# Kernel tuning notes

Measured on AMD Instinct MI355X. Metric: run time of the kernel, lower is better.

Reference implementation:

```python
import jax, jax.numpy as jnp
import numpy as np

B, G, T = 4096, 100, 24


def _greedy_dispatch(demand, caps, prices, slack_price):
    """Exact LP solution of: min prices@alloc + slack_price*slack
    s.t. 0<=alloc<=caps, sum(alloc)+slack = demand (per b,t).
    demand: [B,T] (nonneg), caps: [B,G,T], prices: [G], slack_price: scalar.
    Returns alloc [B,G,T], slack [B,T].
    """
    prices_all = jnp.concatenate([prices, slack_price[None]])        # [G+1]
    # slack capacity = demand itself (slack alone can absorb everything)
    caps_all = jnp.concatenate([caps, demand[:, None, :]], axis=1)    # [B,G+1,T]
    order = jnp.argsort(prices_all)                                   # merit order
    caps_s = caps_all[:, order, :]
    before = jnp.cumsum(caps_s, axis=1) - caps_s                      # capacity ahead in merit order
    alloc_s = jnp.clip(demand[:, None, :] - before, 0.0, caps_s)
    inv = jnp.argsort(order)
    alloc = alloc_s[:, inv, :]
    return alloc[:, :-1, :], alloc[:, -1, :]


def setup_inputs() -> dict:
    key = jax.random.key(0)
    k1, k2, k3, k4 = jax.random.split(key, 4)
    R_up = jax.random.uniform(k1, (B, G, T), dtype=jnp.float32)
    R_dn = jax.random.uniform(k2, (B, G, T), dtype=jnp.float32)
    omega_true = jax.random.normal(k3, (B, T), dtype=jnp.float32) * 5.0
    b_G = 10.0 + 40.0 * jax.random.uniform(k4, (G,), dtype=jnp.float32)  # marginal costs $/MWh
    return {
        "R_up": R_up,
        "R_dn": R_dn,
        "omega_true": omega_true,
        "b_G": b_G,
        "voll": jnp.float32(1000.0),
        "vosp": jnp.float32(500.0),
        "rt_up_ratio": jnp.float32(1.5),
        "rt_dn_ratio": jnp.float32(1.2),
    }


def reference(R_up, R_dn, omega_true, b_G, voll, vosp, rt_up_ratio, rt_dn_ratio):
    c_up = rt_up_ratio * b_G                                          # [G]
    c_dn = rt_dn_ratio * b_G                                          # [G]
    dem_up = jnp.maximum(omega_true, 0.0)                             # [B,T]
    dem_dn = jnp.maximum(-omega_true, 0.0)
    du, LS = _greedy_dispatch(dem_up, R_up, c_up, voll)
    dd, SP = _greedy_dispatch(dem_dn, R_dn, c_dn, vosp)
    rt_obj = (jnp.einsum('g,bgt->b', c_up, du)
              + jnp.einsum('g,bgt->b', c_dn, dd)
              + voll * LS.sum(axis=1) + vosp * SP.sum(axis=1))        # [B]
    return du, dd, LS, SP, rt_obj
```

## Files before the change

### kernel.cpp

```cpp
#include <hip/hip_runtime.h>

#define G_ 100
#define T_ 24
#define GP1 101
#define TILE (G_ * T_)
#define VPB (TILE / 4)
#define BLOCK 256
#define WPB 4

typedef float vfloat4 __attribute__((ext_vector_type(4)));

__global__ void setup_sort_kernel(const float* __restrict__ b_G,
                                  const float* __restrict__ voll,
                                  const float* __restrict__ vosp,
                                  const float* __restrict__ ru,
                                  const float* __restrict__ rd,
                                  int* __restrict__ order_out,
                                  float* __restrict__ price_out)
{
    __shared__ float pu[GP1], pd[GP1];
    int i = threadIdx.x;
    if (i < GP1) {
        if (i < G_) { float bg = b_G[i]; pu[i] = ru[0] * bg; pd[i] = rd[0] * bg; }
        else        { pu[i] = voll[0];   pd[i] = vosp[0]; }
    }
    __syncthreads();
    if (i < GP1) {
        float mu = pu[i], md = pd[i];
        int r0 = 0, r1 = 0;
        for (int j = 0; j < GP1; ++j) {
            float vu = pu[j], vd = pd[j];
            r0 += (vu < mu) || (vu == mu && j < i);
            r1 += (vd < md) || (vd == md && j < i);
        }
        order_out[r0] = i;        price_out[r0] = mu;
        order_out[GP1 + r1] = i;  price_out[GP1 + r1] = md;
    }
}

template<int N>
__device__ __forceinline__ void scan_chunk(int k0,
    float* __restrict__ tile, const int* __restrict__ ordp,
    const float* __restrict__ prp, float dem,
    float& before, float& objp, float& slackv)
{
    int gg[N]; float pr[N], cap[N];
#pragma unroll
    for (int j = 0; j < N; ++j) { gg[j] = ordp[k0 + j]; pr[j] = prp[k0 + j]; }
#pragma unroll
    for (int j = 0; j < N; ++j) {
        int gl = (gg[j] < G_) ? gg[j] : 0;
        cap[j] = tile[gl * T_];
    }
#pragma unroll
    for (int j = 0; j < N; ++j) {
        float c = (gg[j] == G_) ? dem : cap[j];
        float a = fminf(fmaxf(dem - before, 0.f), c);
        before += c;
        objp = fmaf(pr[j], a, objp);
        if (gg[j] == G_) slackv = a;
        else             tile[gg[j] * T_] = a;
    }
}

__global__ __launch_bounds__(BLOCK, 4) void dispatch_kernel(
    const float* __restrict__ R_up, const float* __restrict__ R_dn,
    const float* __restrict__ omega,
    const int* __restrict__ ord_ws, const float* __restrict__ pr_ws,
    float* __restrict__ out, int B)
{
    __shared__ float s_tile[WPB * TILE];

    const int tid  = threadIdx.x;
    const int w    = tid >> 6;
    const int lane = tid & 63;
    const int b    = __builtin_amdgcn_readfirstlane(blockIdx.x * WPB + w);
    const size_t bgt = (size_t)B * TILE;
    float* __restrict__ tw = &s_tile[w * TILE];

    vfloat4 buf[10];
    {
        const vfloat4* __restrict__ s0 = (const vfloat4*)R_up + (size_t)b * VPB;
#pragma unroll
        for (int j = 0; j < 9; ++j) buf[j] = s0[lane + j * 64];
        if (lane < VPB - 576) buf[9] = s0[lane + 576];
    }
    float om = 0.f;
    if (lane < T_) om = omega[(size_t)b * T_ + lane];

    float objsum = 0.f;
#pragma unroll
    for (int p = 0; p < 2; ++p) {
#pragma unroll
        for (int j = 0; j < 9; ++j) *(vfloat4*)&tw[(lane + j * 64) * 4] = buf[j];
        if (lane < VPB - 576)       *(vfloat4*)&tw[(lane + 576) * 4]    = buf[9];
        __builtin_amdgcn_wave_barrier();

        if (p == 0) {
            const vfloat4* __restrict__ s1 = (const vfloat4*)R_dn + (size_t)b * VPB;
#pragma unroll
            for (int j = 0; j < 9; ++j) buf[j] = s1[lane + j * 64];
            if (lane < VPB - 576) buf[9] = s1[lane + 576];
        }

        float objp = 0.f;
        if (lane < T_) {
            const float dem = p ? fmaxf(-om, 0.f) : fmaxf(om, 0.f);
            float* __restrict__ tile = tw + lane;
            const int*   __restrict__ ordp = ord_ws + p * GP1;
            const float* __restrict__ prp  = pr_ws  + p * GP1;
            float before = 0.f, slackv = 0.f;
            scan_chunk<16>( 0, tile, ordp, prp, dem, before, objp, slackv);
            scan_chunk<16>(16, tile, ordp, prp, dem, before, objp, slackv);
            scan_chunk<16>(32, tile, ordp, prp, dem, before, objp, slackv);
            scan_chunk<16>(48, tile, ordp, prp, dem, before, objp, slackv);
            scan_chunk<16>(64, tile, ordp, prp, dem, before, objp, slackv);
            scan_chunk<16>(80, tile, ordp, prp, dem, before, objp, slackv);
            scan_chunk< 5>(96, tile, ordp, prp, dem, before, objp, slackv);
            out[2 * bgt + (size_t)p * B * T_ + (size_t)b * T_ + lane] = slackv;
        }
        __builtin_amdgcn_wave_barrier();

#pragma unroll
        for (int off = 32; off; off >>= 1) objp += __shfl_xor(objp, off, 64);
        objsum += objp;

        {
            vfloat4* __restrict__ dst = (vfloat4*)out + ((size_t)p * B + b) * VPB;
#pragma unroll
            for (int j = 0; j < 9; ++j)
                dst[lane + j * 64] = *(const vfloat4*)&tw[(lane + j * 64) * 4];
            if (lane < VPB - 576)
                dst[lane + 576] = *(const vfloat4*)&tw[(lane + 576) * 4];
        }
        __builtin_amdgcn_wave_barrier();
    }

    if (lane == 0)
        out[2 * bgt + 2 * (size_t)B * T_ + b] = objsum;
}

extern "C" void kernel_launch(void* const* d_in, const int* in_sizes, int n_in,
                              void* d_out, int out_size, void* d_ws, size_t ws_size,
                              hipStream_t stream)
{
    const float* R_up  = (const float*)d_in[0];
    const float* R_dn  = (const float*)d_in[1];
    const float* omega = (const float*)d_in[2];
    const float* b_G   = (const float*)d_in[3];
    const float* voll  = (const float*)d_in[4];
    const float* vosp  = (const float*)d_in[5];
    const float* ru    = (const float*)d_in[6];
    const float* rd    = (const float*)d_in[7];

    const int B = in_sizes[0] / TILE;
    float* out = (float*)d_out;

    int*   ord_ws = (int*)d_ws;
    float* pr_ws  = (float*)((char*)d_ws + 2 * GP1 * sizeof(int));

    setup_sort_kernel<<<1, 128, 0, stream>>>(b_G, voll, vosp, ru, rd, ord_ws, pr_ws);

    dispatch_kernel<<<B / WPB, BLOCK, 0, stream>>>(
        R_up, R_dn, omega, ord_ws, pr_ws, out, B);
}
```

Before: 172.5 us.

## Process up and down dispatch concurrently in one wave per batch

```diff
diff --git a/kernel.cpp b/kernel.cpp
--- a/kernel.cpp
+++ b/kernel.cpp
@@ -5,8 +5,6 @@
 #define GP1 101
 #define TILE (G_ * T_)
 #define VPB (TILE / 4)
-#define BLOCK 256
-#define WPB 4
 
 typedef float vfloat4 __attribute__((ext_vector_type(4)));
 
@@ -40,17 +38,24 @@
 
 template<int N>
 __device__ __forceinline__ void scan_chunk(int k0,
-    float* __restrict__ tile, const int* __restrict__ ordp,
-    const float* __restrict__ prp, float dem,
-    float& before, float& objp, float& slackv)
+    const float* __restrict__ lds, int p, int t,
+    const int* __restrict__ o0, const int* __restrict__ o1,
+    const float* __restrict__ q0, const float* __restrict__ q1,
+    float* __restrict__ dst,
+    float dem, float& before, float& objp, float& slackv)
 {
     int gg[N]; float pr[N], cap[N];
 #pragma unroll
-    for (int j = 0; j < N; ++j) { gg[j] = ordp[k0 + j]; pr[j] = prp[k0 + j]; }
+    for (int j = 0; j < N; ++j) {
+        int ga = o0[k0 + j], gb = o1[k0 + j];
+        float qa = q0[k0 + j], qb = q1[k0 + j];
+        gg[j] = p ? gb : ga;
+        pr[j] = p ? qb : qa;
+    }
 #pragma unroll
     for (int j = 0; j < N; ++j) {
         int gl = (gg[j] < G_) ? gg[j] : 0;
-        cap[j] = tile[gl * T_];
+        cap[j] = lds[p * TILE + gl * T_ + t];
     }
 #pragma unroll
     for (int j = 0; j < N; ++j) {
@@ -59,85 +64,70 @@
         before += c;
         objp = fmaf(pr[j], a, objp);
         if (gg[j] == G_) slackv = a;
-        else             tile[gg[j] * T_] = a;
+        else             dst[gg[j] * T_] = a;
     }
 }
 
-__global__ __launch_bounds__(BLOCK, 4) void dispatch_kernel(
+__global__ __launch_bounds__(64, 2) void dispatch_kernel(
     const float* __restrict__ R_up, const float* __restrict__ R_dn,
     const float* __restrict__ omega,
     const int* __restrict__ ord_ws, const float* __restrict__ pr_ws,
     float* __restrict__ out, int B)
 {
-    __shared__ float s_tile[WPB * TILE];
+    __shared__ float s_tile[2 * TILE];
 
-    const int tid  = threadIdx.x;
-    const int w    = tid >> 6;
-    const int lane = tid & 63;
-    const int b    = __builtin_amdgcn_readfirstlane(blockIdx.x * WPB + w);
+    const int lane = threadIdx.x;
+    const int b    = blockIdx.x;
     const size_t bgt = (size_t)B * TILE;
-    float* __restrict__ tw = &s_tile[w * TILE];
 
-    vfloat4 buf[10];
+    vfloat4 bu[10], bd[10];
     {
         const vfloat4* __restrict__ s0 = (const vfloat4*)R_up + (size_t)b * VPB;
+        const vfloat4* __restrict__ s1 = (const vfloat4*)R_dn + (size_t)b * VPB;
 #pragma unroll
-        for (int j = 0; j < 9; ++j) buf[j] = s0[lane + j * 64];
-        if (lane < VPB - 576) buf[9] = s0[lane + 576];
+        for (int j = 0; j < 9; ++j) { bu[j] = s0[lane + j * 64]; bd[j] = s1[lane + j * 64]; }
+        if (lane < VPB - 576) { bu[9] = s0[lane + 576]; bd[9] = s1[lane + 576]; }
     }
+    const int p = (lane >= T_) ? 1 : 0;
+    const int t = lane - p * T_;
     float om = 0.f;
-    if (lane < T_) om = omega[(size_t)b * T_ + lane];
-
-    float objsum = 0.f;
-#pragma unroll
-    for (int p = 0; p < 2; ++p) {
-#pragma unroll
-        for (int j = 0; j < 9; ++j) *(vfloat4*)&tw[(lane + j * 64) * 4] = buf[j];
-        if (lane < VPB - 576)       *(vfloat4*)&tw[(lane + 576) * 4]    = buf[9];
-        __builtin_amdgcn_wave_barrier();
-
-        if (p == 0) {
-            const vfloat4* __restrict__ s1 = (const vfloat4*)R_dn + (size_t)b * VPB;
-#pragma unroll
-            for (int j = 0; j < 9; ++j) buf[j] = s1[lane + j * 64];
-            if (lane < VPB - 576) buf[9] = s1[lane + 576];
-        }
-
-        float objp = 0.f;
-        if (lane < T_) {
-            const float dem = p ? fmaxf(-om, 0.f) : fmaxf(om, 0.f);
-            float* __restrict__ tile = tw + lane;
-            const int*   __restrict__ ordp = ord_ws + p * GP1;
-            const float* __restrict__ prp  = pr_ws  + p * GP1;
-            float before = 0.f, slackv = 0.f;
-            scan_chunk<16>( 0, tile, ordp, prp, dem, before, objp, slackv);
-            scan_chunk<16>(16, tile, ordp, prp, dem, before, objp, slackv);
-            scan_chunk<16>(32, tile, ordp, prp, dem, before, objp, slackv);
-            scan_chunk<16>(48, tile, ordp, prp, dem, before, objp, slackv);
-            scan_chunk<16>(64, tile, ordp, prp, dem, before, objp, slackv);
-            scan_chunk<16>(80, tile, ordp, prp, dem, before, objp, slackv);
-            scan_chunk< 5>(96, tile, ordp, prp, dem, before, objp, slackv);
-            out[2 * bgt + (size_t)p * B * T_ + (size_t)b * T_ + lane] = slackv;
-        }
-        __builtin_amdgcn_wave_barrier();
+    if (lane < 2 * T_) om = omega[(size_t)b * T_ + t];
 
 #pragma unroll
-        for (int off = 32; off; off >>= 1) objp += __shfl_xor(objp, off, 64);
-        objsum += objp;
+    for (int j = 0; j < 9; ++j) {
+        *(vfloat4*)&s_tile[(lane + j * 64) * 4]        = bu[j];
+        *(vfloat4*)&s_tile[TILE + (lane + j * 64) * 4] = bd[j];
+    }
+    if (lane < VPB - 576) {
+        *(vfloat4*)&s_tile[(lane + 576) * 4]        = bu[9];
+        *(vfloat4*)&s_tile[TILE + (lane + 576) * 4] = bd[9];
+    }
+    __builtin_amdgcn_wave_barrier();
 
-        {
-            vfloat4* __restrict__ dst = (vfloat4*)out + ((size_t)p * B + b) * VPB;
-#pragma unroll
-            for (int j = 0; j < 9; ++j)
-                dst[lane + j * 64] = *(const vfloat4*)&tw[(lane + j * 64) * 4];
-            if (lane < VPB - 576)
-                dst[lane + 576] = *(const vfloat4*)&tw[(lane + 576) * 4];
-        }
-        __builtin_amdgcn_wave_barrier();
+    const int*   __restrict__ o0 = ord_ws;
+    const int*   __restrict__ o1 = ord_ws + GP1;
+    const float* __restrict__ q0 = pr_ws;
+    const float* __restrict__ q1 = pr_ws + GP1;
+
+    float objp = 0.f;
+    if (lane < 2 * T_) {
+        const float dem = p ? fmaxf(-om, 0.f) : fmaxf(om, 0.f);
+        float* __restrict__ dst = out + (size_t)p * bgt + (size_t)b * TILE + t;
+        float before = 0.f, slackv = 0.f;
+        scan_chunk<16>( 0, s_tile, p, t, o0, o1, q0, q1, dst, dem, before, objp, slackv);
+        scan_chunk<16>(16, s_tile, p, t, o0, o1, q0, q1, dst, dem, before, objp, slackv);
+        scan_chunk<16>(32, s_tile, p, t, o0, o1, q0, q1, dst, dem, before, objp, slackv);
+        scan_chunk<16>(48, s_tile, p, t, o0, o1, q0, q1, dst, dem, before, objp, slackv);
+        scan_chunk<16>(64, s_tile, p, t, o0, o1, q0, q1, dst, dem, before, objp, slackv);
+        scan_chunk<16>(80, s_tile, p, t, o0, o1, q0, q1, dst, dem, before, objp, slackv);
+        scan_chunk< 5>(96, s_tile, p, t, o0, o1, q0, q1, dst, dem, before, objp, slackv);
+        out[2 * bgt + (size_t)p * B * T_ + (size_t)b * T_ + t] = slackv;
     }
 
+#pragma unroll
+    for (int off = 32; off; off >>= 1) objp += __shfl_xor(objp, off, 64);
     if (lane == 0)
-        out[2 * bgt + 2 * (size_t)B * T_ + b] = objsum;
+        out[2 * bgt + 2 * (size_t)B * T_ + b] = objp;
 }
 
 extern "C" void kernel_launch(void* const* d_in, const int* in_sizes, int n_in,
@@ -161,6 +151,6 @@
 
     setup_sort_kernel<<<1, 128, 0, stream>>>(b_G, voll, vosp, ru, rd, ord_ws, pr_ws);
 
-    dispatch_kernel<<<B / WPB, BLOCK, 0, stream>>>(
+    dispatch_kernel<<<B, 64, 0, stream>>>(
         R_up, R_dn, omega, ord_ws, pr_ws, out, B);
 }
```

Measured after the change: 172.7 us. About the same (+0.1%).
